# Optimization experiments

Hardware: AMD Instinct MI355X
Metric: run time of the kernel (lower is better)

## Reference

```python
import jax, jax.numpy as jnp
import numpy as np

B, S, H, NH = 2, 2048, 1024, 16
HD = H // NH
BASE = 10000.0


def _rotate_half(x):
    x1, x2 = x[..., : x.shape[-1] // 2], x[..., x.shape[-1] // 2 :]
    return jnp.concatenate((-x2, x1), axis=-1)


def setup_inputs() -> dict:
    key = jax.random.key(0)
    ks = jax.random.split(key, 6)
    hidden_states = jax.random.normal(ks[0], (B, S, H), jnp.float32)
    scale = 0.02
    wq = jax.random.normal(ks[1], (H, H), jnp.float32) * scale
    wk = jax.random.normal(ks[2], (H, H), jnp.float32) * scale
    wv = jax.random.normal(ks[3], (H, H), jnp.float32) * scale
    wo = jax.random.normal(ks[4], (H, H), jnp.float32) * scale
    # additive causal mask, shape (B, 1, S, S): 0 on/below diagonal, large negative above
    neg = jnp.finfo(jnp.float32).min
    causal = jnp.where(jnp.tril(jnp.ones((S, S), dtype=bool)), 0.0, neg).astype(jnp.float32)
    attention_mask = jnp.broadcast_to(causal[None, None], (B, 1, S, S))
    position_ids = jnp.broadcast_to(jnp.arange(S, dtype=jnp.int32)[None], (B, S))
    return {
        "hidden_states": hidden_states,
        "attention_mask": attention_mask,
        "wq": wq,
        "wk": wk,
        "wv": wv,
        "wo": wo,
        "position_ids": position_ids,
    }


def reference(hidden_states, attention_mask, wq, wk, wv, wo, position_ids):
    b, s, h = hidden_states.shape
    dtype = hidden_states.dtype

    def proj(x, w):  # torch Linear: y = x @ w.T, then split heads -> (b, nh, s, hd)
        y = jnp.einsum("bsh,oh->bso", x, w)
        return y.reshape(b, s, NH, HD).transpose(0, 2, 1, 3)

    q = proj(hidden_states, wq)
    k = proj(hidden_states, wk)
    v = proj(hidden_states, wv)

    # rotary cache (computed in fp32 like torch), gathered by position_ids
    inv_freq = 1.0 / (BASE ** (jnp.arange(0, HD, 2, dtype=jnp.float32) / HD))
    t = jnp.arange(s, dtype=jnp.float32)
    freqs = jnp.outer(t, inv_freq)                  # (s, hd/2)
    emb = jnp.concatenate((freqs, freqs), axis=-1)  # (s, hd)
    pos = jnp.clip(position_ids, 0, s - 1)
    cos = jnp.cos(emb).astype(dtype)[pos][:, None]  # (b, 1, s, hd)
    sin = jnp.sin(emb).astype(dtype)[pos][:, None]

    q = q * cos + _rotate_half(q) * sin
    k = k * cos + _rotate_half(k) * sin

    scores = jnp.einsum("bhqd,bhkd->bhqk", q, k) / jnp.sqrt(jnp.asarray(HD, dtype))
    scores = scores + attention_mask
    attn = jax.nn.softmax(scores.astype(jnp.float32), axis=-1).astype(dtype)
    out = jnp.einsum("bhqk,bhkd->bhqd", attn, v)    # (b, nh, s, hd)
    out = out.transpose(0, 2, 1, 3).reshape(b, s, h)
    return jnp.einsum("bso,ho->bsh", out, wo)
```

## Files before the change

kernel.cpp:

```cpp
#include <hip/hip_runtime.h>
#include <cstdint>
#include <cstddef>

typedef unsigned short u16;
typedef __bf16 bf16x8 __attribute__((ext_vector_type(8)));
typedef float f32x4 __attribute__((ext_vector_type(4)));

constexpr int SEQ = 2048;
constexpr int HID = 1024;
constexpr int NHEAD = 16;
constexpr int HDIM = 64;
constexpr int KPAD = 72;

typedef __attribute__((address_space(1))) void gvoid;
typedef __attribute__((address_space(3))) void lvoid;

__device__ __forceinline__ u16 f2bf(float f) {
  union { float f; unsigned u; } v;
  v.f = f;
  unsigned r = v.u + 0x7fffu + ((v.u >> 16) & 1u);
  return (u16)(r >> 16);
}
__device__ __forceinline__ u16 f2bf_trunc(float f) {
  union { float f; unsigned u; } v;
  v.f = f;
  return (u16)(v.u >> 16);
}

__device__ __forceinline__ f32x4 mfma16(bf16x8 a, bf16x8 b, f32x4 c) {
  return __builtin_amdgcn_mfma_f32_16x16x32_bf16(a, b, c, 0, 0, 0);
}

__global__ void detect_kernel(const unsigned* __restrict__ hs, int* __restrict__ flag) {
  unsigned w = hs[threadIdx.x];
  u16 lo = (u16)(w & 0xffffu);
  int e = (lo >> 7) & 0xff;
  bool inr = (e >= 100 && e <= 154);
  unsigned long long m = __ballot(inr);
  if (threadIdx.x == 0) flag[0] = (__popcll(m) >= 48) ? 0 : 1;
}

__global__ __launch_bounds__(256) void cvt_kernel(
    const void* s0, const void* s1, const void* s2, const void* s3, const void* s4,
    u16* __restrict__ d0, u16* __restrict__ d1, u16* __restrict__ d2,
    u16* __restrict__ d3, u16* __restrict__ d4, const int* __restrict__ flag) {
  int b = blockIdx.x;
  const void* s; u16* d; long base;
  if (b < 2048) { s = s0; d = d0; base = (long)b * 2048; }
  else {
    int bb = b - 2048;
    int w = bb >> 9;
    base = (long)(bb & 511) * 2048;
    s = (w == 0) ? s1 : (w == 1) ? s2 : (w == 2) ? s3 : s4;
    d = (w == 0) ? d1 : (w == 1) ? d2 : (w == 2) ? d3 : d4;
  }
  long idx = base + (long)threadIdx.x * 8;
  if (flag[0]) {
    const float* sf = (const float*)s;
    float4 a = *(const float4*)(sf + idx);
    float4 c = *(const float4*)(sf + idx + 4);
    ushort4 p0, p1;
    p0.x = f2bf(a.x); p0.y = f2bf(a.y); p0.z = f2bf(a.z); p0.w = f2bf(a.w);
    p1.x = f2bf(c.x); p1.y = f2bf(c.y); p1.z = f2bf(c.z); p1.w = f2bf(c.w);
    *(ushort4*)(d + idx) = p0;
    *(ushort4*)(d + idx + 4) = p1;
  } else {
    const u16* su = (const u16*)s;
    *(uint4*)(d + idx) = *(const uint4*)(su + idx);
  }
}

__global__ void rope_table_kernel(float* __restrict__ cosb, float* __restrict__ sinb) {
  int idx = blockIdx.x * 256 + threadIdx.x;
  int s = idx >> 5;
  int i = idx & 31;
  float inv_freq = expf(-(float)(2 * i) * (9.210340371976184f / 64.0f));
  float ang = (float)s * inv_freq;
  float c = cosf(ang), sn = sinf(ang);
  cosb[s * 64 + i]      = c;
  cosb[s * 64 + i + 32] = c;
  sinb[s * 64 + i]      = sn;
  sinb[s * 64 + i + 32] = sn;
}

__device__ __forceinline__ void gemm_mainloop_128(
    const u16* __restrict__ Ag, const u16* __restrict__ Bg,
    int row0, int col0, f32x4 acc[4][4]) {
  __shared__ __align__(16) u16 As[128 * 32];
  __shared__ __align__(16) u16 Bs[128 * 32];
  const int t = threadIdx.x;
  const int lane = t & 63, wave = t >> 6;
  const int l15 = lane & 15, quad = lane >> 4;
  const int wm = wave >> 1, wn = wave & 1;
  const int srow = wave * 32 + (lane >> 2);
  const int sg = (lane & 3) * 8;
  u16* ldsA = As + wave * 1024;
  u16* ldsB = Bs + wave * 1024;

  for (int k0 = 0; k0 < 1024; k0 += 32) {
    const u16* ga0 = Ag + (size_t)(row0 + srow) * 1024 + k0 + sg;
    const u16* gb0 = Bg + (size_t)(col0 + srow) * 1024 + k0 + sg;
    __syncthreads();
    __builtin_amdgcn_global_load_lds((gvoid*)ga0,            (lvoid*)ldsA,         16, 0, 0);
    __builtin_amdgcn_global_load_lds((gvoid*)(ga0 + 16384),  (lvoid*)(ldsA + 512), 16, 0, 0);
    __builtin_amdgcn_global_load_lds((gvoid*)gb0,            (lvoid*)ldsB,         16, 0, 0);
    __builtin_amdgcn_global_load_lds((gvoid*)(gb0 + 16384),  (lvoid*)(ldsB + 512), 16, 0, 0);
    __syncthreads();
    bf16x8 af[4], bfr[4];
#pragma unroll
    for (int i = 0; i < 4; i++)
      af[i] = *(const bf16x8*)(As + (wm * 64 + i * 16 + l15) * 32 + quad * 8);
#pragma unroll
    for (int j = 0; j < 4; j++)
      bfr[j] = *(const bf16x8*)(Bs + (wn * 64 + j * 16 + l15) * 32 + quad * 8);
#pragma unroll
    for (int i = 0; i < 4; i++)
#pragma unroll
      for (int j = 0; j < 4; j++)
        acc[i][j] = mfma16(af[i], bfr[j], acc[i][j]);
  }
}

__global__ __launch_bounds__(256) void qkv_kernel(
    const u16* __restrict__ X, const u16* __restrict__ Wq, const u16* __restrict__ Wk,
    const u16* __restrict__ Wv, const int* __restrict__ pos_ids,
    const float* __restrict__ cosb, const float* __restrict__ sinb,
    u16* __restrict__ q_ws, u16* __restrict__ k_ws, u16* __restrict__ vt_ws) {
  const int z = blockIdx.z;
  const u16* Bg = (z == 0) ? Wq : (z == 1) ? Wk : Wv;
  const int row0 = blockIdx.x * 128;
  const int col0 = blockIdx.y * 128;
  f32x4 acc[4][4];
#pragma unroll
  for (int i = 0; i < 4; i++)
#pragma unroll
    for (int j = 0; j < 4; j++) acc[i][j] = f32x4{0.f, 0.f, 0.f, 0.f};

  gemm_mainloop_128(X, Bg, row0, col0, acc);

  const int t = threadIdx.x;
  const int lane = t & 63, wave = t >> 6;
  const int l15 = lane & 15, quad = lane >> 4;
  const int wm = wave >> 1, wn = wave & 1;
  const int gr0 = row0 + wm * 64;
  const int gc0 = col0 + wn * 64;
  const int nh = gc0 >> 6;
  const float qscale = (z == 0) ? 0.18033688011112042f : 1.0f;

  if (z < 2) {
    u16* dst = (z == 0) ? q_ws : k_ws;
#pragma unroll
    for (int i = 0; i < 4; i++) {
#pragma unroll
      for (int r = 0; r < 4; r++) {
        int m = gr0 + i * 16 + quad * 4 + r;
        int b = m >> 11, s = m & 2047;
        int p = pos_ids[m];
        p = min(max(p, 0), SEQ - 1);
#pragma unroll
        for (int j = 0; j < 4; j++) {
          int d = j * 16 + l15;
          float c = cosb[p * 64 + d];
          float sn = sinb[p * 64 + d];
          float v = acc[i][j][r];
          float partner = acc[i][j ^ 2][r];
          float rot = (j < 2) ? -partner : partner;
          float o = (v * c + rot * sn) * qscale;
          dst[((size_t)((b * NHEAD + nh) * SEQ + s) << 6) + d] = f2bf(o);
        }
      }
    }
  } else {
#pragma unroll
    for (int i = 0; i < 4; i++) {
      int m_base = gr0 + i * 16 + quad * 4;
      int b = m_base >> 11, s = m_base & 2047;
#pragma unroll
      for (int j = 0; j < 4; j++) {
        int d = j * 16 + l15;
        ushort4 pk;
        pk.x = f2bf(acc[i][j][0]);
        pk.y = f2bf(acc[i][j][1]);
        pk.z = f2bf(acc[i][j][2]);
        pk.w = f2bf(acc[i][j][3]);
        *(ushort4*)(vt_ws + ((size_t)((b * NHEAD + nh) * 64 + d)) * SEQ + s) = pk;
      }
    }
  }
}

__global__ __launch_bounds__(256) void attn_kernel(
    const u16* __restrict__ q_ws, const u16* __restrict__ k_ws,
    const u16* __restrict__ vt_ws, u16* __restrict__ attn_ws) {
  const int b = blockIdx.z;
  const int x = blockIdx.x;
  const int qt = b ? x : 15 - x;
  const int nh = blockIdx.y;
  const int bh = b * NHEAD + nh;
  __shared__ __align__(16) u16 Ks[2][64 * 64];
  __shared__ __align__(16) u16 Vts[2][64 * 64];
  __shared__ __align__(16) u16 Pl[128 * KPAD];

  const int t = threadIdx.x;
  const int lane = t & 63, wave = t >> 6;
  const int l15 = lane & 15, quad = lane >> 4;
  const int l7 = l15 & 7;
  const int wq0 = qt * 128 + wave * 32;

  bf16x8 aq[2][2];
#pragma unroll
  for (int i = 0; i < 2; i++) {
    const u16* qb = q_ws + ((size_t)bh * SEQ + wq0 + i * 16 + l15) * 64;
    aq[i][0] = *(const bf16x8*)(qb + quad * 8);
    aq[i][1] = *(const bf16x8*)(qb + 32 + quad * 8);
  }

  f32x4 O[2][4];
  float lp[2][4];
#pragma unroll
  for (int i = 0; i < 2; i++)
#pragma unroll
    for (int n = 0; n < 4; n++) { O[i][n] = f32x4{0.f, 0.f, 0.f, 0.f}; lp[i][n] = 0.f; }

  const int rl = (lane >> 3) & 7;
  const int cs = ((lane & 7) ^ rl) * 8;
  const int r16 = wave * 16;
  const u16* kbase = k_ws + (size_t)bh * SEQ * 64;
  const u16* vbase = vt_ws + (size_t)bh * 64 * SEQ;
  const int nkt = 2 * qt + 2;

#define STAGE(ktile, buf)                                                              \
  {                                                                                    \
    u16* ldsK = &Ks[buf][r16 * 64];                                                    \
    u16* ldsV = &Vts[buf][r16 * 64];                                                   \
    const u16* kg = kbase + (size_t)((ktile) * 64 + r16 + rl) * 64 + cs;               \
    const u16* vg = vbase + (size_t)(r16 + rl) * SEQ + (ktile) * 64 + cs;              \
    __builtin_amdgcn_global_load_lds((gvoid*)kg, (lvoid*)ldsK, 16, 0, 0);              \
    __builtin_amdgcn_global_load_lds((gvoid*)(kg + 8 * 64), (lvoid*)(ldsK + 8 * 64),   \
                                     16, 0, 0);                                        \
    __builtin_amdgcn_global_load_lds((gvoid*)vg, (lvoid*)ldsV, 16, 0, 0);              \
    __builtin_amdgcn_global_load_lds((gvoid*)(vg + 8 * SEQ), (lvoid*)(ldsV + 8 * 64),  \
                                     16, 0, 0);                                        \
  }

  STAGE(0, 0)

  for (int kt = 0; kt < nkt; ++kt) {
    const int cur = kt & 1;
    __syncthreads();
    if (kt + 1 < nkt) STAGE(kt + 1, cur ^ 1)
    const u16* Kc = Ks[cur];
    const u16* Vc = Vts[cur];

    f32x4 sc[2][4];
#pragma unroll
    for (int ct = 0; ct < 4; ct++) {
      const int krow = (ct * 16 + l15) * 64;
      bf16x8 bk0 = *(const bf16x8*)(Kc + krow + (quad ^ l7) * 8);
      bf16x8 bk1 = *(const bf16x8*)(Kc + krow + ((quad + 4) ^ l7) * 8);
#pragma unroll
      for (int i = 0; i < 2; i++) {
        f32x4 z4 = f32x4{0.f, 0.f, 0.f, 0.f};
        z4 = mfma16(aq[i][0], bk0, z4);
        z4 = mfma16(aq[i][1], bk1, z4);
        sc[i][ct] = z4;
      }
    }

    if (kt >= 2 * qt) {
#pragma unroll
      for (int i = 0; i < 2; i++) {
        const int qrow = wq0 + i * 16 + quad * 4;
#pragma unroll
        for (int ct = 0; ct < 4; ct++) {
          const int key = kt * 64 + ct * 16 + l15;
#pragma unroll
          for (int r = 0; r < 4; r++) {
            float p = __builtin_amdgcn_exp2f(sc[i][ct][r]);
            if (key > qrow + r) p = 0.f;
            lp[i][r] += p;
            Pl[(wave * 32 + i * 16 + quad * 4 + r) * KPAD + ct * 16 + l15] = f2bf_trunc(p);
          }
        }
      }
    } else {
#pragma unroll
      for (int i = 0; i < 2; i++) {
#pragma unroll
        for (int ct = 0; ct < 4; ct++) {
#pragma unroll
          for (int r = 0; r < 4; r++) {
            float p = __builtin_amdgcn_exp2f(sc[i][ct][r]);
            lp[i][r] += p;
            Pl[(wave * 32 + i * 16 + quad * 4 + r) * KPAD + ct * 16 + l15] = f2bf_trunc(p);
          }
        }
      }
    }

    bf16x8 pa[2][2];
#pragma unroll
    for (int i = 0; i < 2; i++) {
      pa[i][0] = *(const bf16x8*)(Pl + (wave * 32 + i * 16 + l15) * KPAD + quad * 8);
      pa[i][1] = *(const bf16x8*)(Pl + (wave * 32 + i * 16 + l15) * KPAD + 32 + quad * 8);
    }
#pragma unroll
    for (int n = 0; n < 4; n++) {
      const int vrow = (n * 16 + l15) * 64;
      bf16x8 bv0 = *(const bf16x8*)(Vc + vrow + (quad ^ l7) * 8);
      bf16x8 bv1 = *(const bf16x8*)(Vc + vrow + ((quad + 4) ^ l7) * 8);
#pragma unroll
      for (int i = 0; i < 2; i++) {
        O[i][n] = mfma16(pa[i][0], bv0, O[i][n]);
        O[i][n] = mfma16(pa[i][1], bv1, O[i][n]);
      }
    }
  }
#undef STAGE

#pragma unroll
  for (int i = 0; i < 2; i++) {
#pragma unroll
    for (int r = 0; r < 4; r++) {
      float l = lp[i][r];
      l += __shfl_xor(l, 1, 64);
      l += __shfl_xor(l, 2, 64);
      l += __shfl_xor(l, 4, 64);
      l += __shfl_xor(l, 8, 64);
      float inv = 1.0f / l;
      int q = wq0 + i * 16 + quad * 4 + r;
      size_t base = ((size_t)(b * SEQ + q)) * HID + nh * 64;
#pragma unroll
      for (int n = 0; n < 4; n++)
        attn_ws[base + n * 16 + l15] = f2bf(O[i][n][r] * inv);
    }
  }
}

__global__ __launch_bounds__(256) void out_proj_kernel(
    const u16* __restrict__ A, const u16* __restrict__ Wo, void* __restrict__ out,
    const int* __restrict__ flag) {
  const int row0 = blockIdx.x * 128;
  const int col0 = blockIdx.y * 128;
  f32x4 acc[4][4];
#pragma unroll
  for (int i = 0; i < 4; i++)
#pragma unroll
    for (int j = 0; j < 4; j++) acc[i][j] = f32x4{0.f, 0.f, 0.f, 0.f};

  gemm_mainloop_128(A, Wo, row0, col0, acc);

  const int t = threadIdx.x;
  const int lane = t & 63, wave = t >> 6;
  const int l15 = lane & 15, quad = lane >> 4;
  const int wm = wave >> 1, wn = wave & 1;
  const int gr0 = row0 + wm * 64;
  const int gc0 = col0 + wn * 64;
  const bool is_f32 = (flag[0] != 0);
#pragma unroll
  for (int i = 0; i < 4; i++)
#pragma unroll
    for (int r = 0; r < 4; r++) {
      int m = gr0 + i * 16 + quad * 4 + r;
      if (is_f32) {
        float* o = (float*)out;
#pragma unroll
        for (int j = 0; j < 4; j++)
          o[(size_t)m * 1024 + gc0 + j * 16 + l15] = acc[i][j][r];
      } else {
        u16* o = (u16*)out;
#pragma unroll
        for (int j = 0; j < 4; j++)
          o[(size_t)m * 1024 + gc0 + j * 16 + l15] = f2bf(acc[i][j][r]);
      }
    }
}

extern "C" void kernel_launch(void* const* d_in, const int* in_sizes, int n_in,
                              void* d_out, int out_size, void* d_ws, size_t ws_size,
                              hipStream_t stream) {
  const void* hs = d_in[0];
  const void* wq = d_in[2];
  const void* wk = d_in[3];
  const void* wv = d_in[4];
  const void* wo = d_in[5];
  const int* pos = (const int*)d_in[6];

  char* ws = (char*)d_ws;
  float* cosb = (float*)ws;
  float* sinb = (float*)(ws + (512 << 10));
  int* flag   = (int*)(ws + (1020 << 10));
  u16* xbf    = (u16*)(ws + (1 << 20));
  u16* wqbf   = xbf + (size_t)4194304;
  u16* wkbf   = wqbf + (size_t)1048576;
  u16* wvbf   = wkbf + (size_t)1048576;
  u16* wobf   = wvbf + (size_t)1048576;
  u16* q_ws   = wobf + (size_t)1048576;
  u16* k_ws   = q_ws + (size_t)2 * NHEAD * SEQ * HDIM;
  u16* vt_ws  = k_ws + (size_t)2 * NHEAD * SEQ * HDIM;
  u16* attn_ws = vt_ws + (size_t)2 * NHEAD * SEQ * HDIM;

  detect_kernel<<<1, 64, 0, stream>>>((const unsigned*)hs, flag);
  cvt_kernel<<<4096, 256, 0, stream>>>(hs, wq, wk, wv, wo,
                                       xbf, wqbf, wkbf, wvbf, wobf, flag);
  rope_table_kernel<<<256, 256, 0, stream>>>(cosb, sinb);
  qkv_kernel<<<dim3(32, 8, 3), 256, 0, stream>>>(xbf, wqbf, wkbf, wvbf, pos, cosb, sinb,
                                                 q_ws, k_ws, vt_ws);
  attn_kernel<<<dim3(16, NHEAD, 2), 256, 0, stream>>>(q_ws, k_ws, vt_ws, attn_ws);
  out_proj_kernel<<<dim3(32, 8), 256, 0, stream>>>(attn_ws, wobf, d_out, flag);
}
```

Before: 225.4 us.

## Double-buffer GEMM LDS tiles with swizzle, merge rope table into convert kernel

The shared GEMM mainloop now uses two LDS buffers: it prefetches the next K-tile with global_load_lds while computing on the current one, so each iteration needs one barrier instead of two. Columns are XOR-swizzled on write and read to reduce LDS bank conflicts. The three QKV weights are also converted into one concatenated buffer so qkv_kernel runs as a single 2D grid, and the rope table generation is folded into the convert kernel as extra blocks to drop a launch. The risk is that a single barrier may not wait for the asynchronous LDS loads to finish, and the doubled LDS footprint may lower occupancy.

```diff
diff --git a/kernel.cpp b/kernel.cpp
--- a/kernel.cpp
+++ b/kernel.cpp
@@ -42,17 +42,32 @@
 
 __global__ __launch_bounds__(256) void cvt_kernel(
     const void* s0, const void* s1, const void* s2, const void* s3, const void* s4,
-    u16* __restrict__ d0, u16* __restrict__ d1, u16* __restrict__ d2,
-    u16* __restrict__ d3, u16* __restrict__ d4, const int* __restrict__ flag) {
+    u16* __restrict__ d0, u16* __restrict__ dW, const int* __restrict__ flag,
+    float* __restrict__ cosb, float* __restrict__ sinb) {
   int b = blockIdx.x;
+  if (b >= 4096) {
+    int idx = (b - 4096) * 256 + threadIdx.x;
+    int s = idx >> 5;
+    int i = idx & 31;
+    float inv_freq = expf(-(float)(2 * i) * (9.210340371976184f / 64.0f));
+    float ang = (float)s * inv_freq;
+    float c = cosf(ang), sn = sinf(ang);
+    cosb[s * 64 + i]      = c;
+    cosb[s * 64 + i + 32] = c;
+    sinb[s * 64 + i]      = sn;
+    sinb[s * 64 + i + 32] = sn;
+    return;
+  }
   const void* s; u16* d; long base;
   if (b < 2048) { s = s0; d = d0; base = (long)b * 2048; }
   else {
     int bb = b - 2048;
     int w = bb >> 9;
-    base = (long)(bb & 511) * 2048;
+    long src_base = (long)(bb & 511) * 2048;
     s = (w == 0) ? s1 : (w == 1) ? s2 : (w == 2) ? s3 : s4;
-    d = (w == 0) ? d1 : (w == 1) ? d2 : (w == 2) ? d3 : d4;
+    if (w < 3) { d = dW + (long)w * 1048576; base = src_base; }
+    else       { d = dW + (long)3 * 1048576; base = src_base; }
+    base = base;
   }
   long idx = base + (long)threadIdx.x * 8;
   if (flag[0]) {
@@ -70,73 +85,71 @@
   }
 }
 
-__global__ void rope_table_kernel(float* __restrict__ cosb, float* __restrict__ sinb) {
-  int idx = blockIdx.x * 256 + threadIdx.x;
-  int s = idx >> 5;
-  int i = idx & 31;
-  float inv_freq = expf(-(float)(2 * i) * (9.210340371976184f / 64.0f));
-  float ang = (float)s * inv_freq;
-  float c = cosf(ang), sn = sinf(ang);
-  cosb[s * 64 + i]      = c;
-  cosb[s * 64 + i + 32] = c;
-  sinb[s * 64 + i]      = sn;
-  sinb[s * 64 + i + 32] = sn;
-}
-
 __device__ __forceinline__ void gemm_mainloop_128(
     const u16* __restrict__ Ag, const u16* __restrict__ Bg,
     int row0, int col0, f32x4 acc[4][4]) {
-  __shared__ __align__(16) u16 As[128 * 32];
-  __shared__ __align__(16) u16 Bs[128 * 32];
+  __shared__ __align__(16) u16 As[2][128 * 32];
+  __shared__ __align__(16) u16 Bs[2][128 * 32];
   const int t = threadIdx.x;
   const int lane = t & 63, wave = t >> 6;
   const int l15 = lane & 15, quad = lane >> 4;
   const int wm = wave >> 1, wn = wave & 1;
-  const int srow = wave * 32 + (lane >> 2);
-  const int sg = (lane & 3) * 8;
-  u16* ldsA = As + wave * 1024;
-  u16* ldsB = Bs + wave * 1024;
-
-  for (int k0 = 0; k0 < 1024; k0 += 32) {
-    const u16* ga0 = Ag + (size_t)(row0 + srow) * 1024 + k0 + sg;
-    const u16* gb0 = Bg + (size_t)(col0 + srow) * 1024 + k0 + sg;
+  const int lr = lane >> 2;
+  const int cs = ((lane & 3) ^ ((lr >> 1) & 3)) * 8;
+  const u16* arow0 = Ag + (size_t)(row0 + wave * 32 + lr) * 1024 + cs;
+  const u16* arow1 = arow0 + (size_t)16 * 1024;
+  const u16* brow0 = Bg + (size_t)(col0 + wave * 32 + lr) * 1024 + cs;
+  const u16* brow1 = brow0 + (size_t)16 * 1024;
+  const int swz = (quad ^ ((l15 >> 1) & 3)) * 8;
+
+#define GSTAGE(k0, buf)                                                                   \
+  {                                                                                       \
+    u16* la = &As[buf][wave * 1024];                                                      \
+    u16* lb = &Bs[buf][wave * 1024];                                                      \
+    __builtin_amdgcn_global_load_lds((gvoid*)(arow0 + (k0)), (lvoid*)la,         16,0,0); \
+    __builtin_amdgcn_global_load_lds((gvoid*)(arow1 + (k0)), (lvoid*)(la + 512), 16,0,0); \
+    __builtin_amdgcn_global_load_lds((gvoid*)(brow0 + (k0)), (lvoid*)lb,         16,0,0); \
+    __builtin_amdgcn_global_load_lds((gvoid*)(brow1 + (k0)), (lvoid*)(lb + 512), 16,0,0); \
+  }
+
+  GSTAGE(0, 0)
+  for (int kt = 0; kt < 32; ++kt) {
+    const int cur = kt & 1;
     __syncthreads();
-    __builtin_amdgcn_global_load_lds((gvoid*)ga0,            (lvoid*)ldsA,         16, 0, 0);
-    __builtin_amdgcn_global_load_lds((gvoid*)(ga0 + 16384),  (lvoid*)(ldsA + 512), 16, 0, 0);
-    __builtin_amdgcn_global_load_lds((gvoid*)gb0,            (lvoid*)ldsB,         16, 0, 0);
-    __builtin_amdgcn_global_load_lds((gvoid*)(gb0 + 16384),  (lvoid*)(ldsB + 512), 16, 0, 0);
-    __syncthreads();
+    if (kt + 1 < 32) GSTAGE((kt + 1) * 32, cur ^ 1)
+    const u16* Ac = As[cur];
+    const u16* Bc = Bs[cur];
     bf16x8 af[4], bfr[4];
 #pragma unroll
     for (int i = 0; i < 4; i++)
-      af[i] = *(const bf16x8*)(As + (wm * 64 + i * 16 + l15) * 32 + quad * 8);
+      af[i] = *(const bf16x8*)(Ac + (wm * 64 + i * 16 + l15) * 32 + swz);
 #pragma unroll
     for (int j = 0; j < 4; j++)
-      bfr[j] = *(const bf16x8*)(Bs + (wn * 64 + j * 16 + l15) * 32 + quad * 8);
+      bfr[j] = *(const bf16x8*)(Bc + (wn * 64 + j * 16 + l15) * 32 + swz);
 #pragma unroll
     for (int i = 0; i < 4; i++)
 #pragma unroll
       for (int j = 0; j < 4; j++)
         acc[i][j] = mfma16(af[i], bfr[j], acc[i][j]);
   }
+#undef GSTAGE
 }
 
 __global__ __launch_bounds__(256) void qkv_kernel(
-    const u16* __restrict__ X, const u16* __restrict__ Wq, const u16* __restrict__ Wk,
-    const u16* __restrict__ Wv, const int* __restrict__ pos_ids,
+    const u16* __restrict__ X, const u16* __restrict__ Wcat,
+    const int* __restrict__ pos_ids,
     const float* __restrict__ cosb, const float* __restrict__ sinb,
     u16* __restrict__ q_ws, u16* __restrict__ k_ws, u16* __restrict__ vt_ws) {
-  const int z = blockIdx.z;
-  const u16* Bg = (z == 0) ? Wq : (z == 1) ? Wk : Wv;
   const int row0 = blockIdx.x * 128;
   const int col0 = blockIdx.y * 128;
+  const int z = col0 >> 10;
   f32x4 acc[4][4];
 #pragma unroll
   for (int i = 0; i < 4; i++)
 #pragma unroll
     for (int j = 0; j < 4; j++) acc[i][j] = f32x4{0.f, 0.f, 0.f, 0.f};
 
-  gemm_mainloop_128(X, Bg, row0, col0, acc);
+  gemm_mainloop_128(X, Wcat, row0, col0, acc);
 
   const int t = threadIdx.x;
   const int lane = t & 63, wave = t >> 6;
@@ -144,7 +157,7 @@
   const int wm = wave >> 1, wn = wave & 1;
   const int gr0 = row0 + wm * 64;
   const int gc0 = col0 + wn * 64;
-  const int nh = gc0 >> 6;
+  const int nh = (gc0 >> 6) & 15;
   const float qscale = (z == 0) ? 0.18033688011112042f : 1.0f;
 
   if (z < 2) {
@@ -391,21 +404,18 @@
   float* sinb = (float*)(ws + (512 << 10));
   int* flag   = (int*)(ws + (1020 << 10));
   u16* xbf    = (u16*)(ws + (1 << 20));
-  u16* wqbf   = xbf + (size_t)4194304;
-  u16* wkbf   = wqbf + (size_t)1048576;
-  u16* wvbf   = wkbf + (size_t)1048576;
-  u16* wobf   = wvbf + (size_t)1048576;
+  u16* wcat   = xbf + (size_t)4194304;
+  u16* wobf   = wcat + (size_t)3 * 1048576;
   u16* q_ws   = wobf + (size_t)1048576;
   u16* k_ws   = q_ws + (size_t)2 * NHEAD * SEQ * HDIM;
   u16* vt_ws  = k_ws + (size_t)2 * NHEAD * SEQ * HDIM;
   u16* attn_ws = vt_ws + (size_t)2 * NHEAD * SEQ * HDIM;
 
   detect_kernel<<<1, 64, 0, stream>>>((const unsigned*)hs, flag);
-  cvt_kernel<<<4096, 256, 0, stream>>>(hs, wq, wk, wv, wo,
-                                       xbf, wqbf, wkbf, wvbf, wobf, flag);
-  rope_table_kernel<<<256, 256, 0, stream>>>(cosb, sinb);
-  qkv_kernel<<<dim3(32, 8, 3), 256, 0, stream>>>(xbf, wqbf, wkbf, wvbf, pos, cosb, sinb,
-                                                 q_ws, k_ws, vt_ws);
+  cvt_kernel<<<4352, 256, 0, stream>>>(hs, wq, wk, wv, wo, xbf, wcat, flag, cosb, sinb);
+  qkv_kernel<<<dim3(32, 24), 256, 0, stream>>>(xbf, wcat, pos, cosb, sinb,
+                                               q_ws, k_ws, vt_ws);
   attn_kernel<<<dim3(16, NHEAD, 2), 256, 0, stream>>>(q_ws, k_ws, vt_ws, attn_ws);
-  out_proj_kernel<<<dim3(32, 8), 256, 0, stream>>>(attn_ws, wobf, d_out, flag);
-}
+  out_proj_kernel<<<dim3(32, 8), 256, 0, stream>>>(attn_ws, wcat + (size_t)3 * 1048576,
+                                                   d_out, flag);
+}
```

Result: no change. 227.2 us (+0.8%).
